# Optimization experiments

Measured on AMD Instinct MI355X. Metric: run time of the kernel, lower is better.

The kernel has to match this reference:

```python
import jax, jax.numpy as jnp
import numpy as np
from jax import lax

DOWNSAMPLE = 4.0   # downsample_rate
THRESHOLD = 0.7    # score threshold
NMS_RANGE = 3      # maxpool NMS kernel


def setup_inputs() -> dict:
    key = jax.random.key(0)
    k1, k2 = jax.random.split(key)
    radiace_factor = jax.random.uniform(k1, (8, 80, 192, 192), dtype=jnp.float32)  # class heatmap
    box = jax.random.uniform(k2, (8, 4, 192, 192), dtype=jnp.float32)              # [dx, dy, w, h]
    return {"radiace_factor": radiace_factor, "box": box}


def _nms(heat, kernel):
    # max_pool2d(kernel, stride=1, padding=(kernel-1)//2) == SAME window max
    hmax = lax.reduce_window(heat, -jnp.inf, lax.max,
                             (1, 1, kernel, kernel), (1, 1, 1, 1), 'SAME')
    return heat * (hmax == heat).astype(heat.dtype)


def reference(radiace_factor, box):
    B, C, H, W = radiace_factor.shape
    r = jnp.float32(DOWNSAMPLE)

    heat = _nms(radiace_factor, NMS_RANGE)
    score = heat.max(axis=1)               # [B,H,W] max over categories
    mask = score > THRESHOLD               # [B,H,W] kept peaks

    # grid of (x=col, y=row) matching torch.where(inds)[::-1]
    gx, gy = jnp.meshgrid(jnp.arange(W, dtype=jnp.float32),
                          jnp.arange(H, dtype=jnp.float32), indexing='xy')
    grid = jnp.stack([gx, gy], axis=-1)    # [H,W,2]

    b = jnp.moveaxis(box, 1, -1)           # [B,H,W,4] = (dx,dy,w,h)
    center_xy = (grid + b[..., 0:2]) * r   # [B,H,W,2]
    wh = b[..., 2:4] * r

    lim = jnp.array([W * DOWNSAMPLE, H * DOWNSAMPLE], dtype=jnp.float32)
    x1y1 = jnp.clip(center_xy - wh * 0.5, 0.0, lim)
    x2y2 = jnp.clip(center_xy + wh * 0.5, 0.0, lim)
    boxes = jnp.concatenate([x1y1, x2y2 - x1y1], axis=-1)  # [B,H,W,4] (x1,y1,w,h)

    # Dense, jit-friendly equivalent of the per-batch gather: zero-out non-kept
    m = mask[..., None]
    boxes_kept = jnp.where(m, boxes, 0.0)
    scores_kept = jnp.where(mask, score, 0.0)
    center_kept = jnp.where(m, center_xy, 0.0)
    return boxes_kept, mask, scores_kept, center_kept
```

## Files before the change

kernel.cpp:

```cpp
#include <hip/hip_runtime.h>
#include <math.h>


#define BB 8
#define CC 80
#define HH 192
#define WW 192
#define SS 8
#define CG 4
#define CPG (CC/CG)

__global__ __launch_bounds__(256) void score_kernel(const float* __restrict__ heat,
                                                    float* __restrict__ score_out) {
    const int tid  = threadIdx.x;
    const int lane = tid & 63;
    const int wv   = tid >> 6;
    const int xc   = blockIdx.x;
    const int yt   = blockIdx.y;
    const int b    = blockIdx.z;
    const int x0   = xc * 64;
    const int y0   = yt * SS;
    const int x    = x0 + lane;

    __shared__ float red[CG][SS][64];

    float sc[SS];
#pragma unroll
    for (int i = 0; i < SS; ++i) sc[i] = 0.0f;

    const bool haloLane = (lane == 0) || (lane == 63);
    const int  ex   = (lane == 0) ? (x - 1) : (x + 1);
    const bool exok = haloLane && ((unsigned)ex < WW);

    for (int k = 0; k < CPG; ++k) {
        const int c = wv * CPG + k;
        const float* hp = heat + ((size_t)(b * CC + c) * HH) * WW;
        float v[SS + 2], e[SS + 2];
#pragma unroll
        for (int r = 0; r < SS + 2; ++r) {
            const int  row = y0 - 1 + r;
            const bool rok = (unsigned)row < HH;
            v[r] = rok ? hp[row * WW + x] : -INFINITY;
            e[r] = (rok && exok) ? hp[row * WW + ex] : -INFINITY;
        }
        float vm[SS], vme[SS];
#pragma unroll
        for (int i = 0; i < SS; ++i) {
            vm[i]  = fmaxf(fmaxf(v[i], v[i + 1]), v[i + 2]);
            vme[i] = fmaxf(fmaxf(e[i], e[i + 1]), e[i + 2]);
        }
#pragma unroll
        for (int i = 0; i < SS; ++i) {
            float left  = __shfl_up(vm[i], 1);
            float right = __shfl_down(vm[i], 1);
            if (lane == 0)  left  = vme[i];
            if (lane == 63) right = vme[i];
            const float hmax = fmaxf(fmaxf(left, right), vm[i]);
            const float cv   = v[i + 1];
            const float kept = (cv == hmax) ? cv : 0.0f;
            sc[i] = fmaxf(sc[i], kept);
        }
    }

#pragma unroll
    for (int i = 0; i < SS; ++i) red[wv][i][lane] = sc[i];
    __syncthreads();

    for (int j = tid; j < SS * 64; j += 256) {
        const int i = j >> 6, l = j & 63;
        const float m = fmaxf(fmaxf(red[0][i][l], red[1][i][l]),
                              fmaxf(red[2][i][l], red[3][i][l]));
        score_out[((size_t)b * HH + (y0 + i)) * WW + x0 + l] = m;
    }
}

__global__ __launch_bounds__(256) void decode_kernel(const float* __restrict__ box,
                                                     float* __restrict__ out) {
    const int NB  = BB * HH * WW;
    const int pix = blockIdx.x * 256 + threadIdx.x;
    if (pix >= NB) return;

    const int b   = pix / (HH * WW);
    const int rem = pix - b * (HH * WW);
    const int y   = rem / WW;
    const int x   = rem - y * WW;

    float* boxes  = out;
    float* maskp  = out + (size_t)4 * NB;
    float* scorep = out + (size_t)5 * NB;
    float* ctr    = out + (size_t)6 * NB;

    const float s = scorep[pix];
    const bool  m = s > 0.7f;

    const float* bp = box + (size_t)b * 4 * HH * WW + rem;
    const float dx = bp[0];
    const float dy = bp[(size_t)HH * WW];
    const float bw = bp[(size_t)2 * HH * WW];
    const float bh = bp[(size_t)3 * HH * WW];

    const float cx = ((float)x + dx) * 4.0f;
    const float cy = ((float)y + dy) * 4.0f;
    const float w4 = bw * 4.0f;
    const float h4 = bh * 4.0f;
    const float lim = 768.0f;
    const float x1 = fminf(fmaxf(cx - w4 * 0.5f, 0.0f), lim);
    const float y1 = fminf(fmaxf(cy - h4 * 0.5f, 0.0f), lim);
    const float x2 = fminf(fmaxf(cx + w4 * 0.5f, 0.0f), lim);
    const float y2 = fminf(fmaxf(cy + h4 * 0.5f, 0.0f), lim);

    float4 bo;
    bo.x = m ? x1 : 0.0f;
    bo.y = m ? y1 : 0.0f;
    bo.z = m ? (x2 - x1) : 0.0f;
    bo.w = m ? (y2 - y1) : 0.0f;
    reinterpret_cast<float4*>(boxes)[pix] = bo;

    maskp[pix]  = m ? 1.0f : 0.0f;
    scorep[pix] = m ? s : 0.0f;

    float2 cc;
    cc.x = m ? cx : 0.0f;
    cc.y = m ? cy : 0.0f;
    reinterpret_cast<float2*>(ctr)[pix] = cc;
}

extern "C" void kernel_launch(void* const* d_in, const int* in_sizes, int n_in,
                              void* d_out, int out_size, void* d_ws, size_t ws_size,
                              hipStream_t stream) {
    const float* heat = (const float*)d_in[0];
    const float* box  = (const float*)d_in[1];
    float* out = (float*)d_out;
    float* scorep = out + (size_t)5 * BB * HH * WW;

    dim3 g1(WW / 64, HH / SS, BB);
    score_kernel<<<g1, 256, 0, stream>>>(heat, scorep);

    const int NB = BB * HH * WW;
    decode_kernel<<<NB / 256, 256, 0, stream>>>(box, out);
}
```

Baseline: 150.0 us.

## Process full rows with float4 lanes and split channels across two block groups

Each block now covers all 192 columns of an 8-row strip, with 48 lanes each loading float4 vectors. This removes the separate halo-column loads and the per-64-column block tiling. Channels are split into two groups handled by different blocks, which write partial maxima to workspace; the decode kernel combines the two partials. The cost is 16 idle lanes per wave, an extra workspace round trip, and fewer total blocks (384 versus 576).

```diff
diff --git a/kernel.cpp b/kernel.cpp
--- a/kernel.cpp
+++ b/kernel.cpp
@@ -7,78 +7,90 @@
 #define HH 192
 #define WW 192
 #define SS 8
-#define CG 4
-#define CPG (CC/CG)
+#define NBPIX (BB*HH*WW)
 
 __global__ __launch_bounds__(256) void score_kernel(const float* __restrict__ heat,
-                                                    float* __restrict__ score_out) {
+                                                    float* __restrict__ part) {
     const int tid  = threadIdx.x;
     const int lane = tid & 63;
     const int wv   = tid >> 6;
-    const int xc   = blockIdx.x;
-    const int yt   = blockIdx.y;
+    const int yt   = blockIdx.x;
+    const int zs   = blockIdx.y;
     const int b    = blockIdx.z;
-    const int x0   = xc * 64;
     const int y0   = yt * SS;
-    const int x    = x0 + lane;
+    const bool lok = lane < 48;
+    const int  col0 = lane * 4;
 
-    __shared__ float red[CG][SS][64];
+    __shared__ float red[4][SS][WW];
 
-    float sc[SS];
+    float4 sc[SS];
 #pragma unroll
-    for (int i = 0; i < SS; ++i) sc[i] = 0.0f;
+    for (int i = 0; i < SS; ++i) sc[i] = make_float4(0.f, 0.f, 0.f, 0.f);
 
-    const bool haloLane = (lane == 0) || (lane == 63);
-    const int  ex   = (lane == 0) ? (x - 1) : (x + 1);
-    const bool exok = haloLane && ((unsigned)ex < WW);
+    const int cbase = (zs * 4 + wv) * 10;
+    const float NI = -INFINITY;
 
-    for (int k = 0; k < CPG; ++k) {
-        const int c = wv * CPG + k;
+    for (int k = 0; k < 10; ++k) {
+        const int c = cbase + k;
         const float* hp = heat + ((size_t)(b * CC + c) * HH) * WW;
-        float v[SS + 2], e[SS + 2];
+        float4 v[SS + 2];
 #pragma unroll
         for (int r = 0; r < SS + 2; ++r) {
             const int  row = y0 - 1 + r;
-            const bool rok = (unsigned)row < HH;
-            v[r] = rok ? hp[row * WW + x] : -INFINITY;
-            e[r] = (rok && exok) ? hp[row * WW + ex] : -INFINITY;
-        }
-        float vm[SS], vme[SS];
-#pragma unroll
-        for (int i = 0; i < SS; ++i) {
-            vm[i]  = fmaxf(fmaxf(v[i], v[i + 1]), v[i + 2]);
-            vme[i] = fmaxf(fmaxf(e[i], e[i + 1]), e[i + 2]);
+            const bool ok  = lok && ((unsigned)row < HH);
+            v[r] = ok ? *reinterpret_cast<const float4*>(hp + row * WW + col0)
+                      : make_float4(NI, NI, NI, NI);
         }
 #pragma unroll
         for (int i = 0; i < SS; ++i) {
-            float left  = __shfl_up(vm[i], 1);
-            float right = __shfl_down(vm[i], 1);
-            if (lane == 0)  left  = vme[i];
-            if (lane == 63) right = vme[i];
-            const float hmax = fmaxf(fmaxf(left, right), vm[i]);
-            const float cv   = v[i + 1];
-            const float kept = (cv == hmax) ? cv : 0.0f;
-            sc[i] = fmaxf(sc[i], kept);
+            const float4 a = v[i], m = v[i + 1], d = v[i + 2];
+            float4 vm;
+            vm.x = fmaxf(fmaxf(a.x, m.x), d.x);
+            vm.y = fmaxf(fmaxf(a.y, m.y), d.y);
+            vm.z = fmaxf(fmaxf(a.z, m.z), d.z);
+            vm.w = fmaxf(fmaxf(a.w, m.w), d.w);
+
+            float L = __shfl_up(vm.w, 1);
+            float R = __shfl_down(vm.x, 1);
+            if (lane == 0)  L = NI;
+            if (lane >= 47) R = NI;
+
+            float4 hm;
+            hm.x = fmaxf(fmaxf(L,    vm.x), vm.y);
+            hm.y = fmaxf(fmaxf(vm.x, vm.y), vm.z);
+            hm.z = fmaxf(fmaxf(vm.y, vm.z), vm.w);
+            hm.w = fmaxf(fmaxf(vm.z, vm.w), R);
+
+            sc[i].x = fmaxf(sc[i].x, (m.x == hm.x) ? m.x : 0.0f);
+            sc[i].y = fmaxf(sc[i].y, (m.y == hm.y) ? m.y : 0.0f);
+            sc[i].z = fmaxf(sc[i].z, (m.z == hm.z) ? m.z : 0.0f);
+            sc[i].w = fmaxf(sc[i].w, (m.w == hm.w) ? m.w : 0.0f);
         }
     }
 
+    if (lok) {
 #pragma unroll
-    for (int i = 0; i < SS; ++i) red[wv][i][lane] = sc[i];
+        for (int i = 0; i < SS; ++i)
+            *reinterpret_cast<float4*>(&red[wv][i][col0]) = sc[i];
+    }
     __syncthreads();
 
-    for (int j = tid; j < SS * 64; j += 256) {
-        const int i = j >> 6, l = j & 63;
-        const float m = fmaxf(fmaxf(red[0][i][l], red[1][i][l]),
-                              fmaxf(red[2][i][l], red[3][i][l]));
-        score_out[((size_t)b * HH + (y0 + i)) * WW + x0 + l] = m;
+    float* pp = part + ((size_t)(zs * BB + b) * HH + y0) * WW;
+#pragma unroll
+    for (int k = 0; k < SS * WW / 256; ++k) {
+        const int idx = k * 256 + tid;
+        const int row = idx / WW, col = idx - row * WW;
+        const float mx = fmaxf(fmaxf(red[0][row][col], red[1][row][col]),
+                               fmaxf(red[2][row][col], red[3][row][col]));
+        pp[idx] = mx;
     }
 }
 
 __global__ __launch_bounds__(256) void decode_kernel(const float* __restrict__ box,
+                                                     const float* __restrict__ part,
                                                      float* __restrict__ out) {
-    const int NB  = BB * HH * WW;
     const int pix = blockIdx.x * 256 + threadIdx.x;
-    if (pix >= NB) return;
+    if (pix >= NBPIX) return;
 
     const int b   = pix / (HH * WW);
     const int rem = pix - b * (HH * WW);
@@ -86,11 +98,11 @@
     const int x   = rem - y * WW;
 
     float* boxes  = out;
-    float* maskp  = out + (size_t)4 * NB;
-    float* scorep = out + (size_t)5 * NB;
-    float* ctr    = out + (size_t)6 * NB;
+    float* maskp  = out + (size_t)4 * NBPIX;
+    float* scorep = out + (size_t)5 * NBPIX;
+    float* ctr    = out + (size_t)6 * NBPIX;
 
-    const float s = scorep[pix];
+    const float s = fmaxf(part[pix], part[NBPIX + pix]);
     const bool  m = s > 0.7f;
 
     const float* bp = box + (size_t)b * 4 * HH * WW + rem;
@@ -130,12 +142,11 @@
                               hipStream_t stream) {
     const float* heat = (const float*)d_in[0];
     const float* box  = (const float*)d_in[1];
-    float* out = (float*)d_out;
-    float* scorep = out + (size_t)5 * BB * HH * WW;
+    float* out  = (float*)d_out;
+    float* part = (float*)d_ws;
 
-    dim3 g1(WW / 64, HH / SS, BB);
-    score_kernel<<<g1, 256, 0, stream>>>(heat, scorep);
+    dim3 g1(HH / SS, 2, BB);
+    score_kernel<<<g1, 256, 0, stream>>>(heat, part);
 
-    const int NB = BB * HH * WW;
-    decode_kernel<<<NB / 256, 256, 0, stream>>>(box, out);
+    decode_kernel<<<NBPIX / 256, 256, 0, stream>>>(box, part, out);
 }
```

Measured after the change: 148.3 us. No clear change (-1.1%).
